# Kernel optimization log

Measured on AMD Instinct MI355X. Metric: run time of the kernel, lower is better.

## Reference

```python
import jax, jax.numpy as jnp
import numpy as np

COMMITMENT_COST = 0.25
N_EMBED = 1024
EMB_DIM = 256

def setup_inputs() -> dict:
    key = jax.random.key(0)
    k1, k2 = jax.random.split(key)
    z = jax.random.normal(k1, (32, EMB_DIM, 32, 32), dtype=jnp.float32)
    # embedding.weight.data.uniform_(-1/n_embed, 1/n_embed)
    embedding = jax.random.uniform(k2, (N_EMBED, EMB_DIM), dtype=jnp.float32,
                                   minval=-1.0 / N_EMBED, maxval=1.0 / N_EMBED)
    return {"z": z, "embedding": embedding}

def reference(z, embedding):
    # NCHW -> NHWC
    zp = jnp.transpose(z, (0, 2, 3, 1))            # [B,H,W,D]
    in_shape = zp.shape
    flat = zp.reshape(-1, in_shape[-1])            # [N,D]
    # squared L2 distances (argmin equivalent to p=2 cdist argmin)
    d2 = (jnp.sum(flat * flat, axis=1, keepdims=True)
          - 2.0 * (flat @ embedding.T)
          + jnp.sum(embedding * embedding, axis=1))  # [N,K]
    idx = jnp.argmin(d2, axis=1)                   # [N]
    # one-hot @ codebook == direct gather
    z_quant = embedding[idx].reshape(in_shape)     # [B,H,W,D]
    codebook_loss = jnp.mean((z_quant - jax.lax.stop_gradient(zp)) ** 2)
    commitment_loss = jnp.mean((zp - jax.lax.stop_gradient(z_quant)) ** 2)
    loss = codebook_loss + COMMITMENT_COST * commitment_loss
    # straight-through estimator
    z_st = zp + jax.lax.stop_gradient(z_quant - zp)
    z_st = jnp.transpose(z_st, (0, 3, 1, 2))       # NHWC -> NCHW
    return (z_st, loss, codebook_loss, commitment_loss)
```

## Files before the change

kernel.cpp:

```cpp
#include <hip/hip_runtime.h>
#include <hip/hip_bf16.h>
#include <stdint.h>


typedef short v8s __attribute__((ext_vector_type(8)));
typedef float v4f __attribute__((ext_vector_type(4)));

__device__ inline unsigned short f2bf(float f) {
    uint32_t u = __float_as_uint(f);
    return (unsigned short)((u + 0x7fffu + ((u >> 16) & 1u)) >> 16);
}

__global__ __launch_bounds__(256) void k_prep_e(const float* __restrict__ E,
                                                v8s* __restrict__ Esw,
                                                float* __restrict__ nE,
                                                float* __restrict__ accum,
                                                unsigned* __restrict__ done) {
    __shared__ float Ef[16][264];
    int q = blockIdx.x, tid = threadIdx.x;
    const float4* Ein = (const float4*)(E + ((size_t)q << 12));
#pragma unroll
    for (int i = 0; i < 4; i++) {
        int f4 = i * 256 + tid;
        int row = f4 >> 6, c4 = (f4 & 63) << 2;
        *(float4*)&Ef[row][c4] = Ein[f4];
    }
    __syncthreads();
    {
        int c = tid >> 4, l = tid & 15;
        float s = 0.f;
#pragma unroll
        for (int j = 0; j < 16; j++) { float v = Ef[c][l + 16 * j]; s += v * v; }
#pragma unroll
        for (int off = 1; off < 16; off <<= 1) s += __shfl_xor(s, off);
        if (l == 0) nE[q * 16 + c] = 0.5f * s;
    }
#pragma unroll
    for (int i = 0; i < 2; i++) {
        int u = tid + i * 256;
        int um = u & 15, ug = (u >> 4) & 3, udc = (u >> 6) & 7;
        int d0 = udc * 32 + ug * 8;
        union { v8s v; unsigned short s[8]; } pk;
#pragma unroll
        for (int e = 0; e < 8; e++) pk.s[e] = f2bf(Ef[um][d0 + e]);
        Esw[((size_t)q << 9) + u] = pk.v;
    }
    if (q == 0 && tid == 0) { accum[0] = 0.f; done[0] = 0u; }
}

__global__ __launch_bounds__(512, 4) void k_main(
        const v8s* __restrict__ Esw,
        const float* __restrict__ nE,
        const float* __restrict__ z,
        const float* __restrict__ E,
        float* __restrict__ out,
        float* __restrict__ accum,
        unsigned* __restrict__ done) {
    __shared__ union {
        v8s    B[2][2048];
        float4 Eg4[2048];
    } S;
    __shared__ float nEl[1024];
    __shared__ unsigned long long pairLds[64][2];
    __shared__ float nrmLds[64];
    __shared__ int   idxLds[64];

    int tid = threadIdx.x;
    int lane = tid & 63, w = tid >> 6;
    int g = lane >> 4, m = lane & 15;
    int rg = w & 3, h = w >> 2;
    int R0 = blockIdx.x << 6;
    int b = R0 >> 10, hw0 = R0 & 1023;

    {
        int q = tid & 15, dblk = tid >> 4;
        const float* zp = z + ((size_t)b << 18) + hw0 + (q << 2);
        float4 L[8];
#pragma unroll
        for (int j = 0; j < 8; j++)
            L[j] = *(const float4*)(zp + (size_t)(((dblk << 3) + j) << 10));
        const float* Lf = (const float*)L;
#pragma unroll
        for (int c = 0; c < 4; c++) {
            union { v8s v; unsigned short u[8]; } pk;
#pragma unroll
            for (int j = 0; j < 8; j++) pk.u[j] = f2bf(Lf[j * 4 + c]);
            int row = (q << 2) + c;
            int sw = dblk ^ ((row ^ (row >> 2)) & 7);
            *(v8s*)((char*)&S + (row << 9) + (sw << 4)) = pk.v;
        }
    }
#pragma unroll
    for (int i = 0; i < 2; i++) nEl[tid + i * 512] = nE[tid + i * 512];
    __syncthreads();

    v8s a[8];
    {
        int row = (rg << 4) + m;
        int f = (row ^ (row >> 2)) & 7;
#pragma unroll
        for (int dc = 0; dc < 8; dc++) {
            int sw = ((dc << 2) + g) ^ f;
            a[dc] = *(const v8s*)((const char*)&S + (row << 9) + (sw << 4));
        }
        float nrm = 0.f;
#pragma unroll
        for (int dc = 0; dc < 8; dc++) {
            union { v8s v; unsigned short u[8]; } un; un.v = a[dc];
#pragma unroll
            for (int j = 0; j < 8; j++) {
                float v = __uint_as_float((uint32_t)un.u[j] << 16);
                nrm = fmaf(v, v, nrm);
            }
        }
        nrm += __shfl_xor(nrm, 16);
        nrm += __shfl_xor(nrm, 32);
        if (h == 0 && g == 0) nrmLds[row] = nrm;
    }
    __syncthreads();

#define STAGE(ch, buf)                                                        \
    {                                                                         \
        _Pragma("unroll")                                                     \
        for (int j = 0; j < 4; j++) {                                         \
            __builtin_amdgcn_global_load_lds(                                 \
                (const __attribute__((address_space(1))) void*)               \
                    (Esw + ((size_t)(ch) << 11) + (j << 9) + (w << 6) + lane),\
                (__attribute__((address_space(3))) void*)                     \
                    &S.B[buf][(j << 9) + (w << 6)],                           \
                16, 0, 0);                                                    \
        }                                                                     \
    }

    float best[4]; int bidx[4];
#pragma unroll
    for (int r = 0; r < 4; r++) { best[r] = 3.4e38f; bidx[r] = 0; }

    STAGE(0, 0);
#pragma unroll 1
    for (int ct = 0; ct < 16; ct++) {
        int cur = ct & 1;
        __syncthreads();
        if (ct < 15) STAGE(ct + 1, cur ^ 1);
        float ne[2];
#pragma unroll
        for (int t = 0; t < 2; t++) ne[t] = nEl[(ct << 6) + (h << 5) + (t << 4) + m];
        v4f acc[2];
#pragma unroll
        for (int t = 0; t < 2; t++) acc[t] = (v4f){0.f, 0.f, 0.f, 0.f};
#pragma unroll
        for (int dc = 0; dc < 8; dc++) {
#pragma unroll
            for (int t = 0; t < 2; t++) {
                v8s bf = S.B[cur][((h << 1) + t) * 512 + dc * 64 + g * 16 + m];
                acc[t] = __builtin_amdgcn_mfma_f32_16x16x32_bf16(a[dc], bf, acc[t], 0, 0, 0);
            }
        }
#pragma unroll
        for (int t = 0; t < 2; t++) {
            int code = (ct << 6) + (h << 5) + (t << 4) + m;
#pragma unroll
            for (int r = 0; r < 4; r++) {
                float s0 = ne[t] - acc[t][r];
                if (s0 < best[r]) { best[r] = s0; bidx[r] = code; }
            }
        }
    }

#pragma unroll
    for (int r = 0; r < 4; r++) {
        uint32_t sb = __float_as_uint(best[r]);
        sb = (sb & 0x80000000u) ? ~sb : (sb | 0x80000000u);
        unsigned long long pk = ((unsigned long long)sb << 32) | (uint32_t)bidx[r];
#pragma unroll
        for (int off = 1; off < 16; off <<= 1) {
            unsigned long long o = __shfl_xor(pk, off);
            if (o < pk) pk = o;
        }
        if (m == 0)
            pairLds[(rg << 4) + (g << 2) + r][h] = pk;
    }
    __syncthreads();

    float blockLoss = 0.f;
    if (w == 0) {
        unsigned long long p0 = pairLds[lane][0], p1 = pairLds[lane][1];
        unsigned long long pk = p1 < p0 ? p1 : p0;
        idxLds[lane] = (int)(pk & 0xffffffffu);
        uint32_t t = (uint32_t)(pk >> 32);
        float sc = __uint_as_float((t & 0x80000000u) ? (t & 0x7fffffffu) : ~t);
        float ls = 2.0f * sc + nrmLds[lane];
#pragma unroll
        for (int off = 1; off < 64; off <<= 1) ls += __shfl_xor(ls, off);
        blockLoss = ls;
    }
    __syncthreads();

    float* ob = out + ((size_t)b << 18);
    int hwl = tid & 31, dq0 = tid >> 5;
#pragma unroll 1
    for (int ph = 0; ph < 2; ph++) {
#pragma unroll
        for (int i = 0; i < 4; i++) {
            int row = w + (i << 3);
            int k = idxLds[(ph << 5) + row];
            float4 v = ((const float4*)(E + ((size_t)k << 8)))[lane];
            S.Eg4[(row << 6) + (lane ^ row)] = v;
        }
        __syncthreads();
        int hwp = hw0 + (ph << 5) + hwl;
#pragma unroll
        for (int i = 0; i < 4; i++) {
            int dq = dq0 + (i << 4);
            float4 ev = S.Eg4[(hwl << 6) + (dq ^ hwl)];
            size_t o = ((size_t)dq << 12) + hwp;
            ob[o] = ev.x; ob[o + 1024] = ev.y; ob[o + 2048] = ev.z; ob[o + 3072] = ev.w;
        }
        __syncthreads();
    }

    if (tid == 0) {
        atomicAdd(accum, blockLoss);
        __threadfence();
        unsigned old = atomicAdd(done, 1u);
        if (old == 511u) {
            float s = atomicAdd(accum, 0.f) * (1.0f / 8388608.0f);
            out[8388608] = 1.25f * s;
            out[8388609] = s;
            out[8388610] = s;
        }
    }
#undef STAGE
}

extern "C" void kernel_launch(void* const* d_in, const int* in_sizes, int n_in,
                              void* d_out, int out_size, void* d_ws, size_t ws_size,
                              hipStream_t stream) {
    const float* z = (const float*)d_in[0];
    const float* E = (const float*)d_in[1];
    char* ws = (char*)d_ws;
    v8s*      Esw   = (v8s*)(ws);
    float*    nE    = (float*)(ws + 524288);
    float*    accum = (float*)(ws + 528384);
    unsigned* done  = (unsigned*)(ws + 528388);
    float* out = (float*)d_out;

    hipLaunchKernelGGL(k_prep_e, dim3(64),  dim3(256), 0, stream, E, Esw, nE, accum, done);
    hipLaunchKernelGGL(k_main,   dim3(512), dim3(512), 0, stream,
                       Esw, nE, z, E, out, accum, done);
}
```

Baseline: 126.8 us.

## Split codebook across waves and stream B tiles from global into registers

The main kernel moves to 256-thread blocks. Each wave now holds all 64 query rows as four MFMA A-tiles in registers and owns a quarter of the codebook. B fragments are loaded straight from global memory into double-buffered registers, which removes the LDS staging and the per-iteration block barriers. The four per-wave argmin candidates are merged through LDS at the end. The cost is much higher VGPR pressure, which lowers occupancy, and relying on L2 plus a single-step register prefetch to hide global load latency.

```diff
diff --git a/kernel.cpp b/kernel.cpp
--- a/kernel.cpp
+++ b/kernel.cpp
@@ -48,7 +48,7 @@
     if (q == 0 && tid == 0) { accum[0] = 0.f; done[0] = 0u; }
 }
 
-__global__ __launch_bounds__(512, 4) void k_main(
+__global__ __launch_bounds__(256, 2) void k_main(
         const v8s* __restrict__ Esw,
         const float* __restrict__ nE,
         const float* __restrict__ z,
@@ -57,142 +57,148 @@
         float* __restrict__ accum,
         unsigned* __restrict__ done) {
     __shared__ union {
-        v8s    B[2][2048];
+        unsigned char A[32768];
         float4 Eg4[2048];
     } S;
     __shared__ float nEl[1024];
-    __shared__ unsigned long long pairLds[64][2];
+    __shared__ unsigned long long pairLds[64][4];
     __shared__ float nrmLds[64];
     __shared__ int   idxLds[64];
 
     int tid = threadIdx.x;
     int lane = tid & 63, w = tid >> 6;
     int g = lane >> 4, m = lane & 15;
-    int rg = w & 3, h = w >> 2;
     int R0 = blockIdx.x << 6;
     int b = R0 >> 10, hw0 = R0 & 1023;
 
     {
         int q = tid & 15, dblk = tid >> 4;
         const float* zp = z + ((size_t)b << 18) + hw0 + (q << 2);
-        float4 L[8];
-#pragma unroll
-        for (int j = 0; j < 8; j++)
-            L[j] = *(const float4*)(zp + (size_t)(((dblk << 3) + j) << 10));
-        const float* Lf = (const float*)L;
-#pragma unroll
-        for (int c = 0; c < 4; c++) {
-            union { v8s v; unsigned short u[8]; } pk;
-#pragma unroll
-            for (int j = 0; j < 8; j++) pk.u[j] = f2bf(Lf[j * 4 + c]);
-            int row = (q << 2) + c;
-            int sw = dblk ^ ((row ^ (row >> 2)) & 7);
-            *(v8s*)((char*)&S + (row << 9) + (sw << 4)) = pk.v;
-        }
-    }
-#pragma unroll
-    for (int i = 0; i < 2; i++) nEl[tid + i * 512] = nE[tid + i * 512];
-    __syncthreads();
-
-    v8s a[8];
-    {
-        int row = (rg << 4) + m;
-        int f = (row ^ (row >> 2)) & 7;
+#pragma unroll
+        for (int s = 0; s < 2; s++) {
+            float4 L[8];
+#pragma unroll
+            for (int j = 0; j < 8; j++)
+                L[j] = *(const float4*)(zp + (size_t)(((dblk << 4) + (s << 3) + j) << 10));
+            const float* Lf = (const float*)L;
+            int sl = (dblk << 1) + s;
+#pragma unroll
+            for (int c = 0; c < 4; c++) {
+                union { v8s v; unsigned short u[8]; } pk;
+#pragma unroll
+                for (int j = 0; j < 8; j++) pk.u[j] = f2bf(Lf[j * 4 + c]);
+                int r = (q << 2) + c;
+                int sw = sl ^ ((r ^ (r >> 2)) & 7);
+                *(v8s*)(&S.A[(r << 9) + (sw << 4)]) = pk.v;
+            }
+        }
+    }
+#pragma unroll
+    for (int i = 0; i < 4; i++) nEl[tid + (i << 8)] = nE[tid + (i << 8)];
+    __syncthreads();
+
+    v8s a[4][8];
+#pragma unroll
+    for (int mt = 0; mt < 4; mt++) {
+        int r = (mt << 4) + m;
+        int f = (r ^ (r >> 2)) & 7;
 #pragma unroll
         for (int dc = 0; dc < 8; dc++) {
             int sw = ((dc << 2) + g) ^ f;
-            a[dc] = *(const v8s*)((const char*)&S + (row << 9) + (sw << 4));
-        }
-        float nrm = 0.f;
-#pragma unroll
-        for (int dc = 0; dc < 8; dc++) {
-            union { v8s v; unsigned short u[8]; } un; un.v = a[dc];
-#pragma unroll
-            for (int j = 0; j < 8; j++) {
-                float v = __uint_as_float((uint32_t)un.u[j] << 16);
-                nrm = fmaf(v, v, nrm);
-            }
-        }
-        nrm += __shfl_xor(nrm, 16);
-        nrm += __shfl_xor(nrm, 32);
-        if (h == 0 && g == 0) nrmLds[row] = nrm;
-    }
-    __syncthreads();
-
-#define STAGE(ch, buf)                                                        \
-    {                                                                         \
-        _Pragma("unroll")                                                     \
-        for (int j = 0; j < 4; j++) {                                         \
-            __builtin_amdgcn_global_load_lds(                                 \
-                (const __attribute__((address_space(1))) void*)               \
-                    (Esw + ((size_t)(ch) << 11) + (j << 9) + (w << 6) + lane),\
-                (__attribute__((address_space(3))) void*)                     \
-                    &S.B[buf][(j << 9) + (w << 6)],                           \
-                16, 0, 0);                                                    \
-        }                                                                     \
-    }
-
-    float best[4]; int bidx[4];
-#pragma unroll
-    for (int r = 0; r < 4; r++) { best[r] = 3.4e38f; bidx[r] = 0; }
-
-    STAGE(0, 0);
-#pragma unroll 1
+            a[mt][dc] = *(const v8s*)(&S.A[(r << 9) + (sw << 4)]);
+        }
+    }
+    if (w == 0) {
+#pragma unroll
+        for (int mt = 0; mt < 4; mt++) {
+            float nrm = 0.f;
+#pragma unroll
+            for (int dc = 0; dc < 8; dc++) {
+                union { v8s v; unsigned short u[8]; } un; un.v = a[mt][dc];
+#pragma unroll
+                for (int j = 0; j < 8; j++) {
+                    float v = __uint_as_float((uint32_t)un.u[j] << 16);
+                    nrm = fmaf(v, v, nrm);
+                }
+            }
+            nrm += __shfl_xor(nrm, 16);
+            nrm += __shfl_xor(nrm, 32);
+            if (g == 0) nrmLds[(mt << 4) + m] = nrm;
+        }
+    }
+
+    float best[4][4]; int bidx[4][4];
+#pragma unroll
+    for (int mt = 0; mt < 4; mt++)
+#pragma unroll
+        for (int r = 0; r < 4; r++) { best[mt][r] = 3.4e38f; bidx[mt][r] = 0; }
+
+    const v8s* Bq = Esw + ((size_t)(w << 4) << 9) + (g << 4) + m;
+    v8s bb[2][8];
+#pragma unroll
+    for (int dc = 0; dc < 8; dc++) bb[0][dc] = Bq[dc << 6];
+    int c0 = (w << 8) + m;
+#pragma unroll 2
     for (int ct = 0; ct < 16; ct++) {
         int cur = ct & 1;
-        __syncthreads();
-        if (ct < 15) STAGE(ct + 1, cur ^ 1);
-        float ne[2];
-#pragma unroll
-        for (int t = 0; t < 2; t++) ne[t] = nEl[(ct << 6) + (h << 5) + (t << 4) + m];
-        v4f acc[2];
-#pragma unroll
-        for (int t = 0; t < 2; t++) acc[t] = (v4f){0.f, 0.f, 0.f, 0.f};
+        const v8s* Bn = Bq + 512;
+        if (ct < 15) {
+#pragma unroll
+            for (int dc = 0; dc < 8; dc++) bb[cur ^ 1][dc] = Bn[dc << 6];
+        }
+        v4f acc[4];
+#pragma unroll
+        for (int mt = 0; mt < 4; mt++) acc[mt] = (v4f){0.f, 0.f, 0.f, 0.f};
 #pragma unroll
         for (int dc = 0; dc < 8; dc++) {
 #pragma unroll
-            for (int t = 0; t < 2; t++) {
-                v8s bf = S.B[cur][((h << 1) + t) * 512 + dc * 64 + g * 16 + m];
-                acc[t] = __builtin_amdgcn_mfma_f32_16x16x32_bf16(a[dc], bf, acc[t], 0, 0, 0);
-            }
-        }
-#pragma unroll
-        for (int t = 0; t < 2; t++) {
-            int code = (ct << 6) + (h << 5) + (t << 4) + m;
+            for (int mt = 0; mt < 4; mt++)
+                acc[mt] = __builtin_amdgcn_mfma_f32_16x16x32_bf16(
+                              a[mt][dc], bb[cur][dc], acc[mt], 0, 0, 0);
+        }
+        float ne = nEl[c0 + (ct << 4)];
+        int code = c0 + (ct << 4);
+#pragma unroll
+        for (int mt = 0; mt < 4; mt++)
 #pragma unroll
             for (int r = 0; r < 4; r++) {
-                float s0 = ne[t] - acc[t][r];
-                if (s0 < best[r]) { best[r] = s0; bidx[r] = code; }
-            }
-        }
-    }
-
-#pragma unroll
-    for (int r = 0; r < 4; r++) {
-        uint32_t sb = __float_as_uint(best[r]);
-        sb = (sb & 0x80000000u) ? ~sb : (sb | 0x80000000u);
-        unsigned long long pk = ((unsigned long long)sb << 32) | (uint32_t)bidx[r];
-#pragma unroll
-        for (int off = 1; off < 16; off <<= 1) {
-            unsigned long long o = __shfl_xor(pk, off);
+                float s0 = ne - acc[mt][r];
+                if (s0 < best[mt][r]) { best[mt][r] = s0; bidx[mt][r] = code; }
+            }
+        Bq = Bn;
+    }
+
+#pragma unroll
+    for (int mt = 0; mt < 4; mt++)
+#pragma unroll
+        for (int r = 0; r < 4; r++) {
+            uint32_t sb = __float_as_uint(best[mt][r]);
+            sb = (sb & 0x80000000u) ? ~sb : (sb | 0x80000000u);
+            unsigned long long pk = ((unsigned long long)sb << 32) | (uint32_t)bidx[mt][r];
+#pragma unroll
+            for (int off = 1; off < 16; off <<= 1) {
+                unsigned long long o = __shfl_xor(pk, off);
+                if (o < pk) pk = o;
+            }
+            if (m == 0)
+                pairLds[(mt << 4) + (g << 2) + r][w] = pk;
+        }
+    __syncthreads();
+
+    if (tid < 64) {
+        unsigned long long pk = pairLds[tid][0];
+#pragma unroll
+        for (int c = 1; c < 4; c++) {
+            unsigned long long o = pairLds[tid][c];
             if (o < pk) pk = o;
         }
-        if (m == 0)
-            pairLds[(rg << 4) + (g << 2) + r][h] = pk;
-    }
-    __syncthreads();
-
-    float blockLoss = 0.f;
-    if (w == 0) {
-        unsigned long long p0 = pairLds[lane][0], p1 = pairLds[lane][1];
-        unsigned long long pk = p1 < p0 ? p1 : p0;
-        idxLds[lane] = (int)(pk & 0xffffffffu);
+        idxLds[tid] = (int)(pk & 0xffffffffu);
         uint32_t t = (uint32_t)(pk >> 32);
         float sc = __uint_as_float((t & 0x80000000u) ? (t & 0x7fffffffu) : ~t);
-        float ls = 2.0f * sc + nrmLds[lane];
+        float ls = 2.0f * sc + nrmLds[tid];
 #pragma unroll
         for (int off = 1; off < 64; off <<= 1) ls += __shfl_xor(ls, off);
-        blockLoss = ls;
+        if (tid == 0) atomicAdd(accum, ls);
     }
     __syncthreads();
 
@@ -201,8 +207,8 @@
 #pragma unroll 1
     for (int ph = 0; ph < 2; ph++) {
 #pragma unroll
-        for (int i = 0; i < 4; i++) {
-            int row = w + (i << 3);
+        for (int i = 0; i < 8; i++) {
+            int row = (w << 3) + i;
             int k = idxLds[(ph << 5) + row];
             float4 v = ((const float4*)(E + ((size_t)k << 8)))[lane];
             S.Eg4[(row << 6) + (lane ^ row)] = v;
@@ -210,8 +216,8 @@
         __syncthreads();
         int hwp = hw0 + (ph << 5) + hwl;
 #pragma unroll
-        for (int i = 0; i < 4; i++) {
-            int dq = dq0 + (i << 4);
+        for (int i = 0; i < 8; i++) {
+            int dq = (i << 3) + dq0;
             float4 ev = S.Eg4[(hwl << 6) + (dq ^ hwl)];
             size_t o = ((size_t)dq << 12) + hwp;
             ob[o] = ev.x; ob[o + 1024] = ev.y; ob[o + 2048] = ev.z; ob[o + 3072] = ev.w;
@@ -220,7 +226,6 @@
     }
 
     if (tid == 0) {
-        atomicAdd(accum, blockLoss);
         __threadfence();
         unsigned old = atomicAdd(done, 1u);
         if (old == 511u) {
@@ -230,7 +235,6 @@
             out[8388610] = s;
         }
     }
-#undef STAGE
 }
 
 extern "C" void kernel_launch(void* const* d_in, const int* in_sizes, int n_in,
@@ -246,6 +250,6 @@
     float* out = (float*)d_out;
 
     hipLaunchKernelGGL(k_prep_e, dim3(64),  dim3(256), 0, stream, E, Esw, nE, accum, done);
-    hipLaunchKernelGGL(k_main,   dim3(512), dim3(512), 0, stream,
+    hipLaunchKernelGGL(k_main,   dim3(512), dim3(256), 0, stream,
                        Esw, nE, z, E, out, accum, done);
 }
```

After: 138.2 us. +9.0%, slower.
